# Kernel optimization log

Measured on AMD Instinct MI355X. Metric: run time of the kernel, lower is better.

Reference implementation:

```python
import jax, jax.numpy as jnp
import numpy as np


def setup_inputs() -> dict:
    key = jax.random.key(0)
    k1, k2 = jax.random.split(key)
    batch, n = 1024, 32768
    x = jax.random.normal(k1, (batch, 1, n), dtype=jnp.float32)
    activ = jax.random.uniform(k2, (1, n), dtype=jnp.float32)  # EMA buffer state (nonnegative like mean(|x|))
    std = jnp.ones((1,), dtype=jnp.float32)
    return {"x": x, "activ": activ, "std": std}


def reference(x, activ, std):
    batch = x.shape[0]
    # EMA buffer update: activ = 0.97*activ + 0.03*mean(|x|, axis=0)
    activ_new = 0.97 * activ + 0.03 * jnp.mean(jnp.abs(x), axis=0)  # [1, n]
    ac = jnp.exp(-5.0 * jnp.squeeze(activ_new))                      # [n]
    s = jnp.sum(ac)
    ac = ac.at[0].set(s * 4000.0)  # heavily weight index 0 (the "no perturbation" slot)
    # torch.multinomial(ac, batch, replacement=True) == categorical with logits=log(weights)
    r = jax.random.categorical(jax.random.key(42), jnp.log(ac), shape=(batch,))  # [batch] in [0, n)
    i = jnp.arange(batch)
    # x[i, 0, r] += std * (r > 0); (i, r_i) pairs are unique per row so scatter-add == indexed add
    x = x.at[i, 0, r].add(std * (r > 0).astype(x.dtype))
    return x
```

## Files before the change

kernel.cpp:

```cpp
#include <hip/hip_runtime.h>
#include <math.h>

#define NROWS 1024
#define NCOLS 32768
#define NC4   (NCOLS / 4)
#define HCOLS (NCOLS / 2)
#define NB_SCAN 2048
#define KCAND 16
#define TH_BITS 0xFFFC0000u
#define T_GUARD 7.9e-5f

typedef float vfloat4 __attribute__((ext_vector_type(4)));

__device__ __forceinline__ void tf_round(unsigned &x0, unsigned &x1, int r) {
    x0 += x1;
    x1 = __builtin_rotateleft32(x1, r);
    x1 ^= x0;
}

__device__ __forceinline__ void threefry2x32_key0_42(unsigned &x0, unsigned &x1) {
    const unsigned k0 = 0u;
    const unsigned k1 = 42u;
    const unsigned k2 = 0x1BD11BDAu ^ k0 ^ k1;
    x0 += k0; x1 += k1;
    tf_round(x0, x1, 13); tf_round(x0, x1, 15); tf_round(x0, x1, 26); tf_round(x0, x1, 6);
    x0 += k1; x1 += k2 + 1u;
    tf_round(x0, x1, 17); tf_round(x0, x1, 29); tf_round(x0, x1, 16); tf_round(x0, x1, 24);
    x0 += k2; x1 += k0 + 2u;
    tf_round(x0, x1, 13); tf_round(x0, x1, 15); tf_round(x0, x1, 26); tf_round(x0, x1, 6);
    x0 += k0; x1 += k1 + 3u;
    tf_round(x0, x1, 17); tf_round(x0, x1, 29); tf_round(x0, x1, 16); tf_round(x0, x1, 24);
    x0 += k1; x1 += k2 + 4u;
    tf_round(x0, x1, 13); tf_round(x0, x1, 15); tf_round(x0, x1, 26); tf_round(x0, x1, 6);
    x0 += k2; x1 += k0 + 5u;
}

__device__ __forceinline__ float bits_to_u(unsigned bits) {
    float u = __uint_as_float((bits >> 9) | 0x3f800000u) - 1.0f;
    return fmaxf(u, 1.17549435e-38f);
}

__global__ __launch_bounds__(256) void kF(
        const float4* __restrict__ x4, float4* __restrict__ out4,
        float4* __restrict__ partial4, unsigned* __restrict__ bits0,
        unsigned* __restrict__ cnt, uint2* __restrict__ cand,
        int nrb, int stride) {
    const int b = blockIdx.x;
    const int t = threadIdx.x;

    if (b % stride == 0) {
        const int cid = b / stride;
        const int rpb = NROWS / nrb;
        const int bx = cid & 31, by = cid >> 5;
        const int j4 = bx * 256 + t;
        size_t base = (size_t)(by * rpb) * NC4 + j4;
        float4 acc = make_float4(0.f, 0.f, 0.f, 0.f);
        #pragma unroll 8
        for (int r = 0; r < rpb; ++r) {
            float4 v = x4[base];
            vfloat4 nv = { v.x, v.y, v.z, v.w };
            __builtin_nontemporal_store(nv, (vfloat4*)&out4[base]);
            acc.x += fabsf(v.x); acc.y += fabsf(v.y);
            acc.z += fabsf(v.z); acc.w += fabsf(v.w);
            base += NC4;
        }
        partial4[(size_t)by * NC4 + j4] = acc;
    } else {
        const int sid = b - b / stride - 1;
        const int row = sid >> 1, half = sid & 1;
        if (t == 0) cnt[sid] = 0;
        __syncthreads();
        const unsigned cbase = (unsigned)row * (unsigned)NCOLS;
        const int jbase = half * HCOLS;
        #pragma unroll 2
        for (int i = 0; i < HCOLS / 256; ++i) {
            const int j = jbase + (i << 8) + t;
            unsigned x0 = 0u, x1 = cbase + (unsigned)j;
            threefry2x32_key0_42(x0, x1);
            const unsigned bits = x0 ^ x1;
            if (j == 0) {
                bits0[row] = bits;
            } else if (bits >= TH_BITS) {
                unsigned pos = atomicAdd(&cnt[sid], 1u);
                if (pos < KCAND) cand[sid * KCAND + pos] = make_uint2((unsigned)j, bits);
            }
        }
    }
}

__global__ __launch_bounds__(256) void k2_weights(
        const float* __restrict__ partial, const float* __restrict__ activ,
        float* __restrict__ w, float* __restrict__ blocksums,
        float* __restrict__ blockmins, int nrb) {
    const int t = threadIdx.x;
    const int j = blockIdx.x * 256 + t;
    float s = 0.f;
    for (int rb = 0; rb < nrb; ++rb) s += partial[rb * NCOLS + j];
    float m  = s * (1.0f / (float)NROWS);
    float a  = 0.97f * activ[j] + 0.03f * m;
    float ac = expf(-5.0f * a);
    float wj = 1.0f / ac;
    w[j] = wj;
    __shared__ float reds[256];
    __shared__ float redm[256];
    reds[t] = ac;
    redm[t] = (j == 0) ? INFINITY : wj;
    __syncthreads();
    for (int off = 128; off > 0; off >>= 1) {
        if (t < off) {
            reds[t] += reds[t + off];
            redm[t] = fminf(redm[t], redm[t + off]);
        }
        __syncthreads();
    }
    if (t == 0) { blocksums[blockIdx.x] = reds[0]; blockmins[blockIdx.x] = redm[0]; }
}

__global__ __launch_bounds__(64) void k4_resolve(
        const float* __restrict__ w, const float* __restrict__ blocksums,
        const float* __restrict__ blockmins, const unsigned* __restrict__ bits0,
        const unsigned* __restrict__ cnt, const uint2* __restrict__ cand,
        const float* __restrict__ stdp, float* __restrict__ out) {
    const int r = blockIdx.x;
    const int t = threadIdx.x;
    __shared__ float sv[64];
    __shared__ float sm[64];
    __shared__ int   si[64];

    sv[t] = blocksums[t] + blocksums[t + 64];
    sm[t] = fminf(blockmins[t], blockmins[t + 64]);
    __syncthreads();
    for (int off = 32; off > 0; off >>= 1) {
        if (t < off) {
            sv[t] += sv[t + off];
            sm[t] = fminf(sm[t], sm[t + off]);
        }
        __syncthreads();
    }
    const float w0   = 1.0f / (sv[0] * 4000.0f);
    const float wmin = sm[0];

    const float val0 = -__log2f(bits_to_u(bits0[r])) * w0;
    const unsigned c0 = cnt[2 * r];
    const unsigned c1 = cnt[2 * r + 1];
    const bool slow = (c0 > KCAND) || (c1 > KCAND) || !(val0 < T_GUARD * wmin);

    if (!slow) {
        if (t == 0 && (c0 | c1) != 0u) {
            float best = INFINITY;
            int   bi   = 0x7FFFFFFF;
            for (int k = 0; k < (int)c0; ++k) {
                uint2 cd = cand[(2 * r) * KCAND + k];
                float v = -__log2f(bits_to_u(cd.y)) * w[cd.x];
                int   j = (int)cd.x;
                if (v < best || (v == best && j < bi)) { best = v; bi = j; }
            }
            for (int k = 0; k < (int)c1; ++k) {
                uint2 cd = cand[(2 * r + 1) * KCAND + k];
                float v = -__log2f(bits_to_u(cd.y)) * w[cd.x];
                int   j = (int)cd.x;
                if (v < best || (v == best && j < bi)) { best = v; bi = j; }
            }
            if (best < val0 && bi > 0 && bi < NCOLS)
                out[(size_t)r * NCOLS + bi] += stdp[0];
        }
        return;
    }

    const unsigned cbase = (unsigned)r * (unsigned)NCOLS;
    float best = INFINITY;
    int   bi   = 0x7FFFFFFF;
    for (int j = t; j < NCOLS; j += 64) {
        if (j == 0) continue;
        unsigned x0 = 0u, x1 = cbase + (unsigned)j;
        threefry2x32_key0_42(x0, x1);
        float v = -__log2f(bits_to_u(x0 ^ x1)) * w[j];
        if (v < best) { best = v; bi = j; }
    }
    __syncthreads();
    sv[t] = best; si[t] = bi;
    __syncthreads();
    for (int off = 32; off > 0; off >>= 1) {
        if (t < off) {
            float ov = sv[t + off]; int oi = si[t + off];
            if (ov < sv[t] || (ov == sv[t] && oi < si[t])) { sv[t] = ov; si[t] = oi; }
        }
        __syncthreads();
    }
    if (t == 0) {
        if (sv[0] < val0 && si[0] > 0 && si[0] < NCOLS)
            out[(size_t)r * NCOLS + si[0]] += stdp[0];
    }
}

extern "C" void kernel_launch(void* const* d_in, const int* in_sizes, int n_in,
                              void* d_out, int out_size, void* d_ws, size_t ws_size,
                              hipStream_t stream) {
    (void)in_sizes; (void)n_in; (void)out_size;
    const float* x     = (const float*)d_in[0];
    const float* activ = (const float*)d_in[1];
    const float* stdp  = (const float*)d_in[2];
    float* out = (float*)d_out;
    char*  ws  = (char*)d_ws;

    const size_t tail_bytes = (size_t)NCOLS * 4 + 128 * 4 + 128 * 4
                            + NROWS * 4 + (size_t)NB_SCAN * 4
                            + (size_t)NB_SCAN * KCAND * 8;
    int nrb = 16;
    if (ws_size >= (size_t)32 * NCOLS * 4 + tail_bytes) nrb = 32;

    float*    partial   = (float*)ws;
    float*    wbuf      = (float*)(ws + (size_t)nrb * NCOLS * 4);
    float*    blocksums = wbuf + NCOLS;
    float*    blockmins = blocksums + 128;
    unsigned* bits0     = (unsigned*)(blockmins + 128);
    unsigned* cnt       = bits0 + NROWS;
    uint2*    cand      = (uint2*)(cnt + NB_SCAN);

    const int ncopy  = nrb * 32;
    const int stride = (ncopy + NB_SCAN) / ncopy;

    kF<<<ncopy + NB_SCAN, 256, 0, stream>>>((const float4*)x, (float4*)out,
                                            (float4*)partial, bits0, cnt, cand,
                                            nrb, stride);
    k2_weights<<<NCOLS / 256, 256, 0, stream>>>(partial, activ, wbuf,
                                                blocksums, blockmins, nrb);
    k4_resolve<<<NROWS, 64, 0, stream>>>(wbuf, blocksums, blockmins, bits0,
                                         cnt, cand, stdp, out);
}
```

Baseline: 280.3 us.

## Co-schedule copy wave and RNG scan waves within every fused block

Each of the 2048 fused blocks now gives one wavefront to a slice of the copy/abs-sum stream (64 rows by 64 float4 columns) and its other three wavefronts to the threefry candidate scan. Before, whole blocks were dedicated to copying or to scanning. The goal is to overlap memory-bound copy traffic with ALU-bound RNG work inside each CU and to drop the separate copy blocks. The partial-sum count is fixed at 16, and the launch bounds request higher occupancy. In exchange, only one wave per block drives memory traffic, which may reduce bandwidth saturation, and the scan now runs on three waves instead of four.

```diff
diff --git a/kernel.cpp b/kernel.cpp
--- a/kernel.cpp
+++ b/kernel.cpp
@@ -6,6 +6,7 @@
 #define NC4   (NCOLS / 4)
 #define HCOLS (NCOLS / 2)
 #define NB_SCAN 2048
+#define NRB   16
 #define KCAND 16
 #define TH_BITS 0xFFFC0000u
 #define T_GUARD 7.9e-5f
@@ -40,23 +41,28 @@
     return fmaxf(u, 1.17549435e-38f);
 }
 
-__global__ __launch_bounds__(256) void kF(
+__global__ __launch_bounds__(256, 8) void kF(
         const float4* __restrict__ x4, float4* __restrict__ out4,
         float4* __restrict__ partial4, unsigned* __restrict__ bits0,
-        unsigned* __restrict__ cnt, uint2* __restrict__ cand,
-        int nrb, int stride) {
-    const int b = blockIdx.x;
-    const int t = threadIdx.x;
-
-    if (b % stride == 0) {
-        const int cid = b / stride;
-        const int rpb = NROWS / nrb;
-        const int bx = cid & 31, by = cid >> 5;
-        const int j4 = bx * 256 + t;
-        size_t base = (size_t)(by * rpb) * NC4 + j4;
+        unsigned* __restrict__ cnt, uint2* __restrict__ cand) {
+    const int b    = blockIdx.x;
+    const int t    = threadIdx.x;
+    const int wid  = t >> 6;
+    const int lane = t & 63;
+
+    if (t == 0) cnt[b] = 0;
+    __syncthreads();
+
+    const int copy_wid = b & 3;
+
+    if (wid == copy_wid) {
+        const int colg = b & 127;
+        const int rowg = b >> 7;
+        const int j4   = colg * 64 + lane;
+        size_t base = (size_t)(rowg * 64) * NC4 + j4;
         float4 acc = make_float4(0.f, 0.f, 0.f, 0.f);
         #pragma unroll 8
-        for (int r = 0; r < rpb; ++r) {
+        for (int r = 0; r < 64; ++r) {
             float4 v = x4[base];
             vfloat4 nv = { v.x, v.y, v.z, v.w };
             __builtin_nontemporal_store(nv, (vfloat4*)&out4[base]);
@@ -64,25 +70,24 @@
             acc.z += fabsf(v.z); acc.w += fabsf(v.w);
             base += NC4;
         }
-        partial4[(size_t)by * NC4 + j4] = acc;
+        partial4[(size_t)rowg * NC4 + j4] = acc;
     } else {
-        const int sid = b - b / stride - 1;
-        const int row = sid >> 1, half = sid & 1;
-        if (t == 0) cnt[sid] = 0;
-        __syncthreads();
+        const int row  = b >> 1, half = b & 1;
+        const int swid = wid - (wid > copy_wid ? 1 : 0);
+        const int sl   = swid * 64 + lane;
         const unsigned cbase = (unsigned)row * (unsigned)NCOLS;
         const int jbase = half * HCOLS;
-        #pragma unroll 2
-        for (int i = 0; i < HCOLS / 256; ++i) {
-            const int j = jbase + (i << 8) + t;
+        #pragma unroll 4
+        for (int i = sl; i < HCOLS; i += 192) {
+            const int j = jbase + i;
             unsigned x0 = 0u, x1 = cbase + (unsigned)j;
             threefry2x32_key0_42(x0, x1);
             const unsigned bits = x0 ^ x1;
             if (j == 0) {
                 bits0[row] = bits;
             } else if (bits >= TH_BITS) {
-                unsigned pos = atomicAdd(&cnt[sid], 1u);
-                if (pos < KCAND) cand[sid * KCAND + pos] = make_uint2((unsigned)j, bits);
+                unsigned pos = atomicAdd(&cnt[b], 1u);
+                if (pos < KCAND) cand[b * KCAND + pos] = make_uint2((unsigned)j, bits);
             }
         }
     }
@@ -91,11 +96,12 @@
 __global__ __launch_bounds__(256) void k2_weights(
         const float* __restrict__ partial, const float* __restrict__ activ,
         float* __restrict__ w, float* __restrict__ blocksums,
-        float* __restrict__ blockmins, int nrb) {
+        float* __restrict__ blockmins) {
     const int t = threadIdx.x;
     const int j = blockIdx.x * 256 + t;
     float s = 0.f;
-    for (int rb = 0; rb < nrb; ++rb) s += partial[rb * NCOLS + j];
+    #pragma unroll
+    for (int rb = 0; rb < NRB; ++rb) s += partial[rb * NCOLS + j];
     float m  = s * (1.0f / (float)NROWS);
     float a  = 0.97f * activ[j] + 0.03f * m;
     float ac = expf(-5.0f * a);
@@ -196,35 +202,25 @@
 extern "C" void kernel_launch(void* const* d_in, const int* in_sizes, int n_in,
                               void* d_out, int out_size, void* d_ws, size_t ws_size,
                               hipStream_t stream) {
-    (void)in_sizes; (void)n_in; (void)out_size;
+    (void)in_sizes; (void)n_in; (void)out_size; (void)ws_size;
     const float* x     = (const float*)d_in[0];
     const float* activ = (const float*)d_in[1];
     const float* stdp  = (const float*)d_in[2];
     float* out = (float*)d_out;
     char*  ws  = (char*)d_ws;
 
-    const size_t tail_bytes = (size_t)NCOLS * 4 + 128 * 4 + 128 * 4
-                            + NROWS * 4 + (size_t)NB_SCAN * 4
-                            + (size_t)NB_SCAN * KCAND * 8;
-    int nrb = 16;
-    if (ws_size >= (size_t)32 * NCOLS * 4 + tail_bytes) nrb = 32;
-
     float*    partial   = (float*)ws;
-    float*    wbuf      = (float*)(ws + (size_t)nrb * NCOLS * 4);
+    float*    wbuf      = partial + (size_t)NRB * NCOLS;
     float*    blocksums = wbuf + NCOLS;
     float*    blockmins = blocksums + 128;
     unsigned* bits0     = (unsigned*)(blockmins + 128);
     unsigned* cnt       = bits0 + NROWS;
     uint2*    cand      = (uint2*)(cnt + NB_SCAN);
 
-    const int ncopy  = nrb * 32;
-    const int stride = (ncopy + NB_SCAN) / ncopy;
-
-    kF<<<ncopy + NB_SCAN, 256, 0, stream>>>((const float4*)x, (float4*)out,
-                                            (float4*)partial, bits0, cnt, cand,
-                                            nrb, stride);
+    kF<<<NB_SCAN, 256, 0, stream>>>((const float4*)x, (float4*)out,
+                                    (float4*)partial, bits0, cnt, cand);
     k2_weights<<<NCOLS / 256, 256, 0, stream>>>(partial, activ, wbuf,
-                                                blocksums, blockmins, nrb);
+                                                blocksums, blockmins);
     k4_resolve<<<NROWS, 64, 0, stream>>>(wbuf, blocksums, blockmins, bits0,
                                          cnt, cand, stdp, out);
 }
```

After: 254.8 us. -9.1%, faster.
